# Optimization experiments

Measured on AMD Instinct MI355X. Metric: run time of the kernel, lower is better.

The kernel has to match this reference:

```python
import jax, jax.numpy as jnp
import numpy as np

B, S, D_MODEL, D_FORWARD, HEAD = 4, 2048, 1024, 1024, 16
D_K = D_FORWARD // HEAD


def setup_inputs() -> dict:
    key = jax.random.key(0)
    ks = jax.random.split(key, 6)
    scale = 1.0 / np.sqrt(D_MODEL)
    x = jax.random.normal(ks[0], (B, S, D_MODEL), dtype=jnp.float32)
    # per-head projection weights, PyTorch Linear layout [out, in] stacked over heads
    Wq = jax.random.normal(ks[1], (HEAD, D_K, D_MODEL), dtype=jnp.float32) * scale
    Wk = jax.random.normal(ks[2], (HEAD, D_K, D_MODEL), dtype=jnp.float32) * scale
    Wv = jax.random.normal(ks[3], (HEAD, D_K, D_MODEL), dtype=jnp.float32) * scale
    Wo = jax.random.normal(ks[4], (D_MODEL, D_FORWARD), dtype=jnp.float32) * (1.0 / np.sqrt(D_FORWARD))
    bo = jax.random.normal(ks[5], (D_MODEL,), dtype=jnp.float32) * 0.01
    return {"x": x, "Wq": Wq, "Wk": Wk, "Wv": Wv, "Wo": Wo, "bo": bo}


def reference(x, Wq, Wk, Wv, Wo, bo):
    d_k = Wq.shape[1]
    # fused per-head projections: q,k,v are [B, H, S, d_k]
    q = jnp.einsum("bsm,hkm->bhsk", x, Wq)
    k = jnp.einsum("bsm,hkm->bhsk", x, Wk)
    v = jnp.einsum("bsm,hkm->bhsk", x, Wv)
    # raw scores [B, H, S, S]
    scores = jnp.einsum("bhqd,bhkd->bhqk", q, k)
    # custom zero-value mask: entries that are exactly 0 get -1e9
    scores = jnp.where(scores != 0, scores, jnp.float32(-1e9))
    # NOTE: original divides by scale_factor = d_k**-0.5, i.e. multiplies by sqrt(d_k)
    att = jax.nn.softmax(scores * jnp.sqrt(jnp.float32(d_k)), axis=-1)
    z = jnp.einsum("bhqk,bhkd->bhqd", att, v)  # [B, H, S, d_k]
    n_batch, h, s, _ = z.shape
    z = jnp.transpose(z, (0, 2, 1, 3)).reshape(n_batch, s, h * d_k)  # [B, S, d_forward]
    return z @ Wo.T + bo
```

## Files before the change

### kernel.cpp

```cpp
#include <hip/hip_runtime.h>
#include <stdint.h>

typedef __attribute__((ext_vector_type(4))) float f32x4;
typedef __attribute__((ext_vector_type(8))) _Float16 half8;
typedef __attribute__((ext_vector_type(4))) unsigned int u32x4;
typedef __attribute__((ext_vector_type(2))) unsigned int u32x2;

#define MFMA_F16(a, b, c) __builtin_amdgcn_mfma_f32_16x16x32_f16(a, b, c, 0, 0, 0)

#define GLD16(gp, lp)                                                          \
  __builtin_amdgcn_global_load_lds(                                            \
      (const __attribute__((address_space(1))) void*)(gp),                     \
      (__attribute__((address_space(3))) void*)(lp), 16, 0, 0)

__device__ __forceinline__ short f2h(float f) {
  union { _Float16 h; short s; } v;
  v.h = (_Float16)f;
  return v.s;
}
__device__ __forceinline__ float exp2_hw(float x) {
  float r;
  asm("v_exp_f32 %0, %1" : "=v"(r) : "v"(x));
  return r;
}
__device__ __forceinline__ uint32_t pkhf(float lo, float hi) {
  uint32_t r;
  asm("v_cvt_pkrtz_f16_f32 %0, %1, %2" : "=v"(r) : "v"(lo), "v"(hi));
  return r;
}

__global__ __launch_bounds__(256) void cast_all(
    const float* __restrict__ x, const float* __restrict__ wq,
    const float* __restrict__ wk, const float* __restrict__ wv,
    const float* __restrict__ wo, short* __restrict__ Xf,
    short* __restrict__ Wf, short* __restrict__ Wof) {
  const int bid = blockIdx.x;
  const float* src;
  short* dst;
  int lb;
  if (bid < 8192) {
    src = x; dst = Xf; lb = bid;
  } else if (bid < 9216) {
    src = wq; dst = Wf; lb = bid - 8192;
  } else if (bid < 10240) {
    src = wk; dst = Wf + 1048576; lb = bid - 9216;
  } else if (bid < 11264) {
    src = wv; dst = Wf + 2097152; lb = bid - 10240;
  } else {
    src = wo; dst = Wof; lb = bid - 11264;
  }
  const size_t i = (size_t)lb * 256 + threadIdx.x;
  f32x4 v = *reinterpret_cast<const f32x4*>(src + i * 4);
  u32x2 o;
  o[0] = pkhf(v[0], v[1]);
  o[1] = pkhf(v[2], v[3]);
  *reinterpret_cast<u32x2*>(dst + i * 4) = o;
}

__global__ __launch_bounds__(256) void gemm_proj(
    const short* __restrict__ Xf, const short* __restrict__ Wf,
    short* __restrict__ Qf, short* __restrict__ Kf, short* __restrict__ Vt) {
  __shared__ short sA[128 * 64], sB[128 * 64];
  const int tid = threadIdx.x, lane = tid & 63, w = tid >> 6;
  const int wr = w >> 1, wc = w & 1;
  const int g = lane >> 4, c = lane & 15;
  const int L = blockIdx.x;
  const int xcd = L & 7, idx = L >> 3;
  const int xcol = xcd * 3 + (idx % 3);
  const int yrow = idx / 3;
  const int m0 = yrow * 128, n0 = xcol * 128;

  f32x4 acc[4][4];
#pragma unroll
  for (int i = 0; i < 4; i++)
#pragma unroll
    for (int j = 0; j < 4; j++) acc[i][j] = (f32x4){0.f, 0.f, 0.f, 0.f};

  const int sw0 = ((0 * 4 + g) ^ (c & 7)) * 8;
  const int sw1 = ((1 * 4 + g) ^ (c & 7)) * 8;

  for (int ks = 0; ks < 16; ks++) {
    const int k0 = ks * 64;
    __syncthreads();
#pragma unroll
    for (int i = 0; i < 4; i++) {
      const int ch = i * 256 + tid;
      const int row = ch >> 3;
      const int colg = (ch & 7) ^ (row & 7);
      const size_t aoff = (size_t)(m0 + row) * 1024 + k0 + colg * 8;
      const size_t boff = (size_t)(n0 + row) * 1024 + k0 + colg * 8;
      GLD16(Xf + aoff, (char*)sA + ch * 16);
      GLD16(Wf + boff, (char*)sB + ch * 16);
    }
    asm volatile("s_waitcnt vmcnt(0)" ::: "memory");
    __syncthreads();

#pragma unroll
    for (int cc = 0; cc < 2; cc++) {
      const int sw = cc ? sw1 : sw0;
      half8 a[4], b8[4];
#pragma unroll
      for (int i = 0; i < 4; i++) {
        a[i] = *(const half8*)&sA[(wr * 64 + i * 16 + c) * 64 + sw];
        b8[i] = *(const half8*)&sB[(wc * 64 + i * 16 + c) * 64 + sw];
      }
#pragma unroll
      for (int i = 0; i < 4; i++)
#pragma unroll
        for (int j = 0; j < 4; j++)
          acc[i][j] = MFMA_F16(a[i], b8[j], acc[i][j]);
    }
  }

  const int section = n0 >> 10;
#pragma unroll
  for (int i = 0; i < 4; i++)
#pragma unroll
    for (int j = 0; j < 4; j++)
#pragma unroll
      for (int r = 0; r < 4; r++) {
        const float v = acc[i][j][r];
        const int m = m0 + wr * 64 + i * 16 + g * 4 + r;
        const int n = n0 + wc * 64 + j * 16 + c;
        const int b = m >> 11, s = m & 2047;
        const int nn = n & 1023;
        const int hh = nn >> 6, d = nn & 63;
        if (section == 0) {
          const size_t off = ((size_t)(b * 16 + hh) * 2048 + s) * 64 + d;
          Qf[off] = f2h(v * 11.5415603271f);
        } else if (section == 1) {
          const size_t off = ((size_t)(b * 16 + hh) * 2048 + s) * 64 + d;
          Kf[off] = f2h(v);
        } else {
          Vt[((size_t)(b * 16 + hh) * 64 + d) * 2048 + s] = f2h(v);
        }
      }
}

__global__ __launch_bounds__(256, 4) void attn_kernel(
    const short* __restrict__ Qf, const short* __restrict__ Kf,
    const short* __restrict__ Vt, short* __restrict__ Z) {
  __shared__ short sK[2][64 * 64];
  __shared__ short sV[2][64 * 64];
  const int tid = threadIdx.x, lane = tid & 63, w = tid >> 6;
  const int g = lane >> 4, c = lane & 15;
  const int L = blockIdx.x;
  const int wid = (L & 7) * 128 + (L >> 3);
  const int qblk = wid & 15, bh = wid >> 4;
  const int b = bh >> 4, h = bh & 15;
  const size_t base = (size_t)bh * (2048 * 64);

  half8 qf[2][2];
  {
    const int qrow = qblk * 128 + w * 32 + c;
#pragma unroll
    for (int qi = 0; qi < 2; qi++)
#pragma unroll
      for (int cc = 0; cc < 2; cc++) {
        const size_t off =
            base + (size_t)(qrow + qi * 16) * 64 + cc * 32 + g * 8;
        qf[qi][cc] = *(const half8*)(Qf + off);
      }
  }

  f32x4 zacc[2][4];
  f32x4 lacc[2];
  float m_run[2] = {-INFINITY, -INFINITY};
#pragma unroll
  for (int qi = 0; qi < 2; qi++) {
    lacc[qi] = (f32x4){0.f, 0.f, 0.f, 0.f};
#pragma unroll
    for (int dt = 0; dt < 4; dt++) zacc[qi][dt] = (f32x4){0.f, 0.f, 0.f, 0.f};
  }

  half8 ones;
#pragma unroll
  for (int i = 0; i < 8; i++) ones[i] = (_Float16)1.0f;

  const int sw0 = ((0 * 4 + g) ^ (c & 7)) * 8;
  const int sw1 = ((1 * 4 + g) ^ (c & 7)) * 8;

  const int ch0 = tid, ch1 = tid + 256;
  const int kr0 = ch0 >> 3, kc0 = (ch0 & 7) ^ (kr0 & 7);
  const int kr1 = ch1 >> 3, kc1 = (ch1 & 7) ^ (kr1 & 7);
  const int kofs0 = kr0 * 64 + kc0 * 8, kofs1 = kr1 * 64 + kc1 * 8;
  const int vofs0 = kr0 * 2048 + kc0 * 8, vofs1 = kr1 * 2048 + kc1 * 8;
  const int ldo0 = ch0 * 16, ldo1 = ch1 * 16;

  auto stage = [&](int buf, int kt) {
    const size_t kb = base + (size_t)kt * 4096;
    const size_t vb = base + (size_t)kt * 64;
    GLD16(Kf + kb + kofs0, (char*)&sK[buf][0] + ldo0);
    GLD16(Kf + kb + kofs1, (char*)&sK[buf][0] + ldo1);
    GLD16(Vt + vb + vofs0, (char*)&sV[buf][0] + ldo0);
    GLD16(Vt + vb + vofs1, (char*)&sV[buf][0] + ldo1);
  };

  const int srcl = ((g & 1) << 5) + c;

  auto compute = [&](int buf) {
    f32x4 sacc[2][4];
#pragma unroll
    for (int qi = 0; qi < 2; qi++)
#pragma unroll
      for (int t = 0; t < 4; t++) sacc[qi][t] = (f32x4){0.f, 0.f, 0.f, 0.f};
    __builtin_amdgcn_s_setprio(1);
#pragma unroll
    for (int cc = 0; cc < 2; cc++) {
      const int sw = cc ? sw1 : sw0;
#pragma unroll
      for (int t = 0; t < 4; t++) {
        const int kr = (t * 16 + c) * 64 + sw;
        half8 k8 = *(const half8*)&sK[buf][kr];
        sacc[0][t] = MFMA_F16(k8, qf[0][cc], sacc[0][t]);
        sacc[1][t] = MFMA_F16(k8, qf[1][cc], sacc[1][t]);
      }
    }
    __builtin_amdgcn_s_setprio(0);

    float p0[16], p1[16];
#pragma unroll
    for (int t = 0; t < 4; t++)
#pragma unroll
      for (int r = 0; r < 4; r++) {
        p0[t * 4 + r] = sacc[0][t][r];
        p1[t * 4 + r] = sacc[1][t][r];
      }
    float mx0, mx1;
    {
      float m = fmaxf(p0[0], p0[1]);
      m = fmaxf(fmaxf(m, p0[2]), p0[3]);
      m = fmaxf(fmaxf(m, p0[4]), p0[5]);
      m = fmaxf(fmaxf(m, p0[6]), p0[7]);
      m = fmaxf(fmaxf(m, p0[8]), p0[9]);
      m = fmaxf(fmaxf(m, p0[10]), p0[11]);
      m = fmaxf(fmaxf(m, p0[12]), p0[13]);
      m = fmaxf(fmaxf(m, p0[14]), p0[15]);
      m = fmaxf(m, __shfl_xor(m, 16));
      mx0 = fmaxf(m, __shfl_xor(m, 32));
    }
    {
      float m = fmaxf(p1[0], p1[1]);
      m = fmaxf(fmaxf(m, p1[2]), p1[3]);
      m = fmaxf(fmaxf(m, p1[4]), p1[5]);
      m = fmaxf(fmaxf(m, p1[6]), p1[7]);
      m = fmaxf(fmaxf(m, p1[8]), p1[9]);
      m = fmaxf(fmaxf(m, p1[10]), p1[11]);
      m = fmaxf(fmaxf(m, p1[12]), p1[13]);
      m = fmaxf(fmaxf(m, p1[14]), p1[15]);
      m = fmaxf(m, __shfl_xor(m, 16));
      mx1 = fmaxf(m, __shfl_xor(m, 32));
    }
    const float growmax = fmaxf(mx0 - m_run[0], mx1 - m_run[1]);
    if (!__any(growmax > -20.0f)) return;
    if (__any(growmax > 8.0f)) {
#pragma unroll
      for (int qi = 0; qi < 2; qi++) {
        const float mnew = fmaxf(m_run[qi], qi ? mx1 : mx0);
        const float sc = exp2_hw(m_run[qi] - mnew);
        m_run[qi] = mnew;
#pragma unroll
        for (int r = 0; r < 4; r++) lacc[qi][r] *= sc;
#pragma unroll
        for (int dt = 0; dt < 4; dt++)
#pragma unroll
          for (int r = 0; r < 4; r++) zacc[qi][dt][r] *= sc;
      }
    }
#pragma unroll
    for (int i = 0; i < 16; i++) {
      p0[i] = exp2_hw(p0[i] - m_run[0]);
      p1[i] = exp2_hw(p1[i] - m_run[1]);
    }

    union { u32x4 u; half8 s; } pfa0, pfa1, pfb0, pfb1;
    {
      const uint32_t wA0 = pkhf(p0[0], p0[1]), wA1 = pkhf(p0[2], p0[3]);
      const uint32_t wB0 = pkhf(p0[4], p0[5]), wB1 = pkhf(p0[6], p0[7]);
      const uint32_t a0 = __shfl(wA0, srcl), a1 = __shfl(wA1, srcl);
      const uint32_t b0 = __shfl(wB0, srcl), b1 = __shfl(wB1, srcl);
      const uint32_t a2 = __shfl(wA0, srcl + 16), a3 = __shfl(wA1, srcl + 16);
      const uint32_t b2 = __shfl(wB0, srcl + 16), b3 = __shfl(wB1, srcl + 16);
      pfa0.u[0] = (g < 2) ? a0 : b0;
      pfa0.u[1] = (g < 2) ? a1 : b1;
      pfa0.u[2] = (g < 2) ? a2 : b2;
      pfa0.u[3] = (g < 2) ? a3 : b3;
    }
    {
      const uint32_t wA0 = pkhf(p0[8], p0[9]), wA1 = pkhf(p0[10], p0[11]);
      const uint32_t wB0 = pkhf(p0[12], p0[13]), wB1 = pkhf(p0[14], p0[15]);
      const uint32_t a0 = __shfl(wA0, srcl), a1 = __shfl(wA1, srcl);
      const uint32_t b0 = __shfl(wB0, srcl), b1 = __shfl(wB1, srcl);
      const uint32_t a2 = __shfl(wA0, srcl + 16), a3 = __shfl(wA1, srcl + 16);
      const uint32_t b2 = __shfl(wB0, srcl + 16), b3 = __shfl(wB1, srcl + 16);
      pfa1.u[0] = (g < 2) ? a0 : b0;
      pfa1.u[1] = (g < 2) ? a1 : b1;
      pfa1.u[2] = (g < 2) ? a2 : b2;
      pfa1.u[3] = (g < 2) ? a3 : b3;
    }
    {
      const uint32_t wA0 = pkhf(p1[0], p1[1]), wA1 = pkhf(p1[2], p1[3]);
      const uint32_t wB0 = pkhf(p1[4], p1[5]), wB1 = pkhf(p1[6], p1[7]);
      const uint32_t a0 = __shfl(wA0, srcl), a1 = __shfl(wA1, srcl);
      const uint32_t b0 = __shfl(wB0, srcl), b1 = __shfl(wB1, srcl);
      const uint32_t a2 = __shfl(wA0, srcl + 16), a3 = __shfl(wA1, srcl + 16);
      const uint32_t b2 = __shfl(wB0, srcl + 16), b3 = __shfl(wB1, srcl + 16);
      pfb0.u[0] = (g < 2) ? a0 : b0;
      pfb0.u[1] = (g < 2) ? a1 : b1;
      pfb0.u[2] = (g < 2) ? a2 : b2;
      pfb0.u[3] = (g < 2) ? a3 : b3;
    }
    {
      const uint32_t wA0 = pkhf(p1[8], p1[9]), wA1 = pkhf(p1[10], p1[11]);
      const uint32_t wB0 = pkhf(p1[12], p1[13]), wB1 = pkhf(p1[14], p1[15]);
      const uint32_t a0 = __shfl(wA0, srcl), a1 = __shfl(wA1, srcl);
      const uint32_t b0 = __shfl(wB0, srcl), b1 = __shfl(wB1, srcl);
      const uint32_t a2 = __shfl(wA0, srcl + 16), a3 = __shfl(wA1, srcl + 16);
      const uint32_t b2 = __shfl(wB0, srcl + 16), b3 = __shfl(wB1, srcl + 16);
      pfb1.u[0] = (g < 2) ? a0 : b0;
      pfb1.u[1] = (g < 2) ? a1 : b1;
      pfb1.u[2] = (g < 2) ? a2 : b2;
      pfb1.u[3] = (g < 2) ? a3 : b3;
    }

    __builtin_amdgcn_s_setprio(1);
    lacc[0] = MFMA_F16(ones, pfa0.s, lacc[0]);
    lacc[0] = MFMA_F16(ones, pfa1.s, lacc[0]);
    lacc[1] = MFMA_F16(ones, pfb0.s, lacc[1]);
    lacc[1] = MFMA_F16(ones, pfb1.s, lacc[1]);
#pragma unroll
    for (int dt = 0; dt < 4; dt++) {
      const int vr = (dt * 16 + c) * 64;
      half8 vb0 = *(const half8*)&sV[buf][vr + sw0];
      half8 vb1 = *(const half8*)&sV[buf][vr + sw1];
      zacc[0][dt] = MFMA_F16(vb0, pfa0.s, zacc[0][dt]);
      zacc[0][dt] = MFMA_F16(vb1, pfa1.s, zacc[0][dt]);
      zacc[1][dt] = MFMA_F16(vb0, pfb0.s, zacc[1][dt]);
      zacc[1][dt] = MFMA_F16(vb1, pfb1.s, zacc[1][dt]);
    }
    __builtin_amdgcn_s_setprio(0);
  };

  stage(0, 0);
  asm volatile("s_waitcnt vmcnt(0)" ::: "memory");
  __builtin_amdgcn_s_barrier();

#pragma unroll 1
  for (int t2 = 0; t2 < 16; t2++) {
    {
      stage(1, 2 * t2 + 1);
      compute(0);
      asm volatile("s_waitcnt vmcnt(0) lgkmcnt(0)" ::: "memory");
      __builtin_amdgcn_s_barrier();
    }
    {
      const int nxt = 2 * t2 + 2;
      stage(0, nxt < 32 ? nxt : 31);
      compute(1);
      asm volatile("s_waitcnt vmcnt(0) lgkmcnt(0)" ::: "memory");
      __builtin_amdgcn_s_barrier();
    }
  }

  const int qg0 = qblk * 128 + w * 32 + c;
#pragma unroll
  for (int qi = 0; qi < 2; qi++) {
    const float rs = lacc[qi][0];
    const float inv = rs > 0.f ? 1.0f / rs : 0.f;
    const int qg = qg0 + qi * 16;
#pragma unroll
    for (int dt = 0; dt < 4; dt++) {
      u32x2 zw;
      zw[0] = pkhf(zacc[qi][dt][0] * inv, zacc[qi][dt][1] * inv);
      zw[1] = pkhf(zacc[qi][dt][2] * inv, zacc[qi][dt][3] * inv);
      *reinterpret_cast<u32x2*>(
          &Z[(size_t)(b * 2048 + qg) * 1024 + h * 64 + dt * 16 + g * 4]) = zw;
    }
  }
}

__global__ __launch_bounds__(256) void gemm_out(
    const short* __restrict__ Zb, const short* __restrict__ Wof,
    const float* __restrict__ bo, float* __restrict__ out) {
  __shared__ short sA[128 * 64], sB[128 * 64];
  const int tid = threadIdx.x, lane = tid & 63, w = tid >> 6;
  const int wr = w >> 1, wc = w & 1;
  const int g = lane >> 4, c = lane & 15;
  const int L = blockIdx.x;
  const int m0 = (L >> 3) * 128, n0 = (L & 7) * 128;

  f32x4 acc[4][4];
#pragma unroll
  for (int i = 0; i < 4; i++)
#pragma unroll
    for (int j = 0; j < 4; j++) acc[i][j] = (f32x4){0.f, 0.f, 0.f, 0.f};

  const int sw0 = ((0 * 4 + g) ^ (c & 7)) * 8;
  const int sw1 = ((1 * 4 + g) ^ (c & 7)) * 8;

  for (int ks = 0; ks < 16; ks++) {
    const int k0 = ks * 64;
    __syncthreads();
#pragma unroll
    for (int i = 0; i < 4; i++) {
      const int ch = i * 256 + tid;
      const int row = ch >> 3;
      const int colg = (ch & 7) ^ (row & 7);
      const size_t aoff = (size_t)(m0 + row) * 1024 + k0 + colg * 8;
      const size_t boff = (size_t)(n0 + row) * 1024 + k0 + colg * 8;
      GLD16(Zb + aoff, (char*)sA + ch * 16);
      GLD16(Wof + boff, (char*)sB + ch * 16);
    }
    asm volatile("s_waitcnt vmcnt(0)" ::: "memory");
    __syncthreads();

#pragma unroll
    for (int cc = 0; cc < 2; cc++) {
      const int sw = cc ? sw1 : sw0;
      half8 a[4], b8[4];
#pragma unroll
      for (int i = 0; i < 4; i++) {
        a[i] = *(const half8*)&sA[(wr * 64 + i * 16 + c) * 64 + sw];
        b8[i] = *(const half8*)&sB[(wc * 64 + i * 16 + c) * 64 + sw];
      }
#pragma unroll
      for (int i = 0; i < 4; i++)
#pragma unroll
        for (int j = 0; j < 4; j++)
          acc[i][j] = MFMA_F16(a[i], b8[j], acc[i][j]);
    }
  }

#pragma unroll
  for (int i = 0; i < 4; i++)
#pragma unroll
    for (int j = 0; j < 4; j++)
#pragma unroll
      for (int r = 0; r < 4; r++) {
        const int m = m0 + wr * 64 + i * 16 + g * 4 + r;
        const int n = n0 + wc * 64 + j * 16 + c;
        out[(size_t)m * 1024 + n] = acc[i][j][r] + bo[n];
      }
}

extern "C" void kernel_launch(void* const* d_in, const int* in_sizes, int n_in,
                              void* d_out, int out_size, void* d_ws, size_t ws_size,
                              hipStream_t stream) {
  const float* x  = (const float*)d_in[0];
  const float* Wq = (const float*)d_in[1];
  const float* Wk = (const float*)d_in[2];
  const float* Wv = (const float*)d_in[3];
  const float* Wo = (const float*)d_in[4];
  const float* bo = (const float*)d_in[5];
  float* out = (float*)d_out;

  const size_t NX = 8388608;
  const size_t NW = 1048576;
  const size_t NQ = 8388608;

  char* p = (char*)d_ws;
  auto take = [&](size_t bytes) -> char* {
    char* r = p;
    p += (bytes + 255) & ~(size_t)255;
    return r;
  };
  short* Xf  = (short*)take(NX * 2);
  short* Wf  = (short*)take(3 * NW * 2);
  short* Wof = (short*)take(NW * 2);
  short* Qf  = (short*)take(NQ * 2);
  short* Kf  = (short*)take(NQ * 2);
  short* Vt  = (short*)take(NQ * 2);
  short* Zb  = (short*)take(NQ * 2);

  cast_all<<<dim3(12288), 256, 0, stream>>>(x, Wq, Wk, Wv, Wo, Xf, Wf, Wof);
  gemm_proj<<<dim3(1536), 256, 0, stream>>>(Xf, Wf, Qf, Kf, Vt);
  attn_kernel<<<dim3(1024), 256, 0, stream>>>(Qf, Kf, Vt, Zb);
  gemm_out<<<dim3(512), 256, 0, stream>>>(Zb, Wof, bo, out);
}
```

Measured before the change: 238.5 us.

## Feed P directly to 16x16x16 MFMA, dropping cross-lane shuffles; defer row-max reduction

The PV and row-sum products now use the 16x16x16 f16 MFMA, so the score accumulator layout can serve directly as the B operand. This removes the 32 cross-lane shuffles per tile that repacked P for the 16x16x32 instruction, and V fragments are read as 4-wide halves at matching swizzled offsets. The row-max cross-lane reduction now only runs when a rescale is needed; the skip test uses per-lane maxima. The cost is twice as many MFMA instructions at half the K depth, and more, narrower LDS reads of V.

```diff
diff --git a/kernel.cpp b/kernel.cpp
--- a/kernel.cpp
+++ b/kernel.cpp
@@ -3,10 +3,11 @@
 
 typedef __attribute__((ext_vector_type(4))) float f32x4;
 typedef __attribute__((ext_vector_type(8))) _Float16 half8;
-typedef __attribute__((ext_vector_type(4))) unsigned int u32x4;
+typedef __attribute__((ext_vector_type(4))) _Float16 half4;
 typedef __attribute__((ext_vector_type(2))) unsigned int u32x2;
 
 #define MFMA_F16(a, b, c) __builtin_amdgcn_mfma_f32_16x16x32_f16(a, b, c, 0, 0, 0)
+#define MFMA16(a, b, c) __builtin_amdgcn_mfma_f32_16x16x16f16(a, b, c, 0, 0, 0)
 
 #define GLD16(gp, lp)                                                          \
   __builtin_amdgcn_global_load_lds(                                            \
@@ -173,9 +174,9 @@
     for (int dt = 0; dt < 4; dt++) zacc[qi][dt] = (f32x4){0.f, 0.f, 0.f, 0.f};
   }
 
-  half8 ones;
-#pragma unroll
-  for (int i = 0; i < 8; i++) ones[i] = (_Float16)1.0f;
+  half4 ones4;
+#pragma unroll
+  for (int i = 0; i < 4; i++) ones4[i] = (_Float16)1.0f;
 
   const int sw0 = ((0 * 4 + g) ^ (c & 7)) * 8;
   const int sw1 = ((1 * 4 + g) ^ (c & 7)) * 8;
@@ -196,8 +197,6 @@
     GLD16(Vt + vb + vofs1, (char*)&sV[buf][0] + ldo1);
   };
 
-  const int srcl = ((g & 1) << 5) + c;
-
   auto compute = [&](int buf) {
     f32x4 sacc[2][4];
 #pragma unroll
@@ -226,7 +225,7 @@
         p0[t * 4 + r] = sacc[0][t][r];
         p1[t * 4 + r] = sacc[1][t][r];
       }
-    float mx0, mx1;
+    float mxl0, mxl1;
     {
       float m = fmaxf(p0[0], p0[1]);
       m = fmaxf(fmaxf(m, p0[2]), p0[3]);
@@ -235,9 +234,7 @@
       m = fmaxf(fmaxf(m, p0[8]), p0[9]);
       m = fmaxf(fmaxf(m, p0[10]), p0[11]);
       m = fmaxf(fmaxf(m, p0[12]), p0[13]);
-      m = fmaxf(fmaxf(m, p0[14]), p0[15]);
-      m = fmaxf(m, __shfl_xor(m, 16));
-      mx0 = fmaxf(m, __shfl_xor(m, 32));
+      mxl0 = fmaxf(fmaxf(m, p0[14]), p0[15]);
     }
     {
       float m = fmaxf(p1[0], p1[1]);
@@ -247,13 +244,15 @@
       m = fmaxf(fmaxf(m, p1[8]), p1[9]);
       m = fmaxf(fmaxf(m, p1[10]), p1[11]);
       m = fmaxf(fmaxf(m, p1[12]), p1[13]);
-      m = fmaxf(fmaxf(m, p1[14]), p1[15]);
-      m = fmaxf(m, __shfl_xor(m, 16));
-      mx1 = fmaxf(m, __shfl_xor(m, 32));
-    }
-    const float growmax = fmaxf(mx0 - m_run[0], mx1 - m_run[1]);
-    if (!__any(growmax > -20.0f)) return;
-    if (__any(growmax > 8.0f)) {
+      mxl1 = fmaxf(fmaxf(m, p1[14]), p1[15]);
+    }
+    const float grow = fmaxf(mxl0 - m_run[0], mxl1 - m_run[1]);
+    if (!__any(grow > -20.0f)) return;
+    if (__any(grow > 8.0f)) {
+      float mx0 = fmaxf(mxl0, __shfl_xor(mxl0, 16));
+      mx0 = fmaxf(mx0, __shfl_xor(mx0, 32));
+      float mx1 = fmaxf(mxl1, __shfl_xor(mxl1, 16));
+      mx1 = fmaxf(mx1, __shfl_xor(mx1, 32));
 #pragma unroll
       for (int qi = 0; qi < 2; qi++) {
         const float mnew = fmaxf(m_run[qi], qi ? mx1 : mx0);
@@ -273,70 +272,23 @@
       p1[i] = exp2_hw(p1[i] - m_run[1]);
     }
 
-    union { u32x4 u; half8 s; } pfa0, pfa1, pfb0, pfb1;
-    {
-      const uint32_t wA0 = pkhf(p0[0], p0[1]), wA1 = pkhf(p0[2], p0[3]);
-      const uint32_t wB0 = pkhf(p0[4], p0[5]), wB1 = pkhf(p0[6], p0[7]);
-      const uint32_t a0 = __shfl(wA0, srcl), a1 = __shfl(wA1, srcl);
-      const uint32_t b0 = __shfl(wB0, srcl), b1 = __shfl(wB1, srcl);
-      const uint32_t a2 = __shfl(wA0, srcl + 16), a3 = __shfl(wA1, srcl + 16);
-      const uint32_t b2 = __shfl(wB0, srcl + 16), b3 = __shfl(wB1, srcl + 16);
-      pfa0.u[0] = (g < 2) ? a0 : b0;
-      pfa0.u[1] = (g < 2) ? a1 : b1;
-      pfa0.u[2] = (g < 2) ? a2 : b2;
-      pfa0.u[3] = (g < 2) ? a3 : b3;
-    }
-    {
-      const uint32_t wA0 = pkhf(p0[8], p0[9]), wA1 = pkhf(p0[10], p0[11]);
-      const uint32_t wB0 = pkhf(p0[12], p0[13]), wB1 = pkhf(p0[14], p0[15]);
-      const uint32_t a0 = __shfl(wA0, srcl), a1 = __shfl(wA1, srcl);
-      const uint32_t b0 = __shfl(wB0, srcl), b1 = __shfl(wB1, srcl);
-      const uint32_t a2 = __shfl(wA0, srcl + 16), a3 = __shfl(wA1, srcl + 16);
-      const uint32_t b2 = __shfl(wB0, srcl + 16), b3 = __shfl(wB1, srcl + 16);
-      pfa1.u[0] = (g < 2) ? a0 : b0;
-      pfa1.u[1] = (g < 2) ? a1 : b1;
-      pfa1.u[2] = (g < 2) ? a2 : b2;
-      pfa1.u[3] = (g < 2) ? a3 : b3;
-    }
-    {
-      const uint32_t wA0 = pkhf(p1[0], p1[1]), wA1 = pkhf(p1[2], p1[3]);
-      const uint32_t wB0 = pkhf(p1[4], p1[5]), wB1 = pkhf(p1[6], p1[7]);
-      const uint32_t a0 = __shfl(wA0, srcl), a1 = __shfl(wA1, srcl);
-      const uint32_t b0 = __shfl(wB0, srcl), b1 = __shfl(wB1, srcl);
-      const uint32_t a2 = __shfl(wA0, srcl + 16), a3 = __shfl(wA1, srcl + 16);
-      const uint32_t b2 = __shfl(wB0, srcl + 16), b3 = __shfl(wB1, srcl + 16);
-      pfb0.u[0] = (g < 2) ? a0 : b0;
-      pfb0.u[1] = (g < 2) ? a1 : b1;
-      pfb0.u[2] = (g < 2) ? a2 : b2;
-      pfb0.u[3] = (g < 2) ? a3 : b3;
-    }
-    {
-      const uint32_t wA0 = pkhf(p1[8], p1[9]), wA1 = pkhf(p1[10], p1[11]);
-      const uint32_t wB0 = pkhf(p1[12], p1[13]), wB1 = pkhf(p1[14], p1[15]);
-      const uint32_t a0 = __shfl(wA0, srcl), a1 = __shfl(wA1, srcl);
-      const uint32_t b0 = __shfl(wB0, srcl), b1 = __shfl(wB1, srcl);
-      const uint32_t a2 = __shfl(wA0, srcl + 16), a3 = __shfl(wA1, srcl + 16);
-      const uint32_t b2 = __shfl(wB0, srcl + 16), b3 = __shfl(wB1, srcl + 16);
-      pfb1.u[0] = (g < 2) ? a0 : b0;
-      pfb1.u[1] = (g < 2) ? a1 : b1;
-      pfb1.u[2] = (g < 2) ? a2 : b2;
-      pfb1.u[3] = (g < 2) ? a3 : b3;
-    }
-
     __builtin_amdgcn_s_setprio(1);
-    lacc[0] = MFMA_F16(ones, pfa0.s, lacc[0]);
-    lacc[0] = MFMA_F16(ones, pfa1.s, lacc[0]);
-    lacc[1] = MFMA_F16(ones, pfb0.s, lacc[1]);
-    lacc[1] = MFMA_F16(ones, pfb1.s, lacc[1]);
-#pragma unroll
-    for (int dt = 0; dt < 4; dt++) {
-      const int vr = (dt * 16 + c) * 64;
-      half8 vb0 = *(const half8*)&sV[buf][vr + sw0];
-      half8 vb1 = *(const half8*)&sV[buf][vr + sw1];
-      zacc[0][dt] = MFMA_F16(vb0, pfa0.s, zacc[0][dt]);
-      zacc[0][dt] = MFMA_F16(vb1, pfa1.s, zacc[0][dt]);
-      zacc[1][dt] = MFMA_F16(vb0, pfb0.s, zacc[1][dt]);
-      zacc[1][dt] = MFMA_F16(vb1, pfb1.s, zacc[1][dt]);
+#pragma unroll
+    for (int t = 0; t < 4; t++) {
+      union { u32x2 u; half4 h; } b0, b1;
+      b0.u[0] = pkhf(p0[4 * t + 0], p0[4 * t + 1]);
+      b0.u[1] = pkhf(p0[4 * t + 2], p0[4 * t + 3]);
+      b1.u[0] = pkhf(p1[4 * t + 0], p1[4 * t + 1]);
+      b1.u[1] = pkhf(p1[4 * t + 2], p1[4 * t + 3]);
+      lacc[0] = MFMA16(ones4, b0.h, lacc[0]);
+      lacc[1] = MFMA16(ones4, b1.h, lacc[1]);
+      const int vo = ((2 * t + (g >> 1)) ^ (c & 7)) * 8 + (g & 1) * 4;
+#pragma unroll
+      for (int dt = 0; dt < 4; dt++) {
+        half4 va = *(const half4*)&sV[buf][(dt * 16 + c) * 64 + vo];
+        zacc[0][dt] = MFMA16(va, b0.h, zacc[0][dt]);
+        zacc[1][dt] = MFMA16(va, b1.h, zacc[1][dt]);
+      }
     }
     __builtin_amdgcn_s_setprio(0);
   };
```

After: 232.8 us, median of 2. -2.4%, faster.
